# Kernel optimization log

Hardware: AMD Instinct MI355X
Metric: run time of the kernel (lower is better)

The kernel has to match this reference:

```python
import jax, jax.numpy as jnp
import numpy as np

B, H, S, D = 2, 16, 2048, 64
DROPOUT_P = 0.1
INV_SCALE = 8.0  # sqrt(D), original: q.size(3) * k.size(-1)**-0.5


def setup_inputs() -> dict:
    key = jax.random.key(0)
    kq, kk, kv, km = jax.random.split(key, 4)
    query = jax.random.normal(kq, (B, H, S, D), dtype=jnp.float32)
    k_ = jax.random.normal(kk, (B, H, S, D), dtype=jnp.float32)
    value = jax.random.normal(kv, (B, H, S, D), dtype=jnp.float32)
    keep = jax.random.bernoulli(km, 1.0 - DROPOUT_P, (B, H, S, S))
    # torch train-mode dropout: keep-mask scaled by 1/(1-p)
    dropout_mask = keep.astype(jnp.float32) / (1.0 - DROPOUT_P)
    return {"query": query, "key": k_, "value": value, "dropout_mask": dropout_mask}


def reference(query, key, value, dropout_mask):
    # qk = q @ k^T, scaled by 1/sqrt(D)
    scores = jnp.einsum("bhqd,bhkd->bhqk", query, key) / INV_SCALE
    probs = jax.nn.softmax(scores, axis=-1)
    probs = probs * dropout_mask  # deterministic dropout
    out = jnp.einsum("bhqk,bhkd->bhqd", probs, value)
    return out
```

## Files before the change

kernel.cpp:

```cpp
#include <hip/hip_runtime.h>
#include <hip/hip_bf16.h>

typedef __attribute__((ext_vector_type(4))) float f32x4;
typedef __attribute__((ext_vector_type(8))) short s16x8;
typedef __attribute__((ext_vector_type(4))) short s16x4;

constexpr int S    = 2048;
constexpr int D    = 64;
constexpr int BH   = 32;
constexpr int QBLK = 64;
constexpr int KBLK = 32;
constexpr int NSL  = S / KBLK;

__device__ __forceinline__ short f2bf(float f) {
  union { float f; unsigned u; } x;
  x.f = f;
  unsigned r = x.u + 0x7fffu + ((x.u >> 16) & 1u);
  return (short)(r >> 16);
}

typedef const __attribute__((address_space(1))) unsigned int* as1_u32p;
typedef __attribute__((address_space(3))) unsigned int* as3_u32p;

__global__ __launch_bounds__(256) void prepass(const float* __restrict__ K,
                                               const float* __restrict__ V,
                                               short* __restrict__ Kb,
                                               short* __restrict__ Vt) {
  const int bid = blockIdx.x;
  const int tid = threadIdx.x;
  if (bid < BH * 32) {
    const int bh = bid >> 5, sl = bid & 31;
    const float* src = K + ((size_t)bh * S + (size_t)sl * 64) * D;
    short* dst = Kb + ((size_t)bh * S + (size_t)sl * 64) * D;
    #pragma unroll
    for (int c = 0; c < 2; ++c) {
      const int idx = tid * 2 + c;
      const int row = idx >> 3;
      const int ch  = idx & 7;
      const float* s = src + row * D + ch * 8;
      f32x4 a = *(const f32x4*)s, b = *(const f32x4*)(s + 4);
      s16x8 o;
      #pragma unroll
      for (int j = 0; j < 4; ++j) { o[j] = f2bf(a[j]); o[4 + j] = f2bf(b[j]); }
      *(s16x8*)(dst + row * D + ((ch ^ (row & 7)) * 8)) = o;
    }
  } else {
    __shared__ short tile[32][72];
    const int b2 = bid - BH * 32;
    const int bh = b2 >> 6, sl = b2 & 63;
    const float* src = V + ((size_t)bh * S + (size_t)sl * 32) * D;
    {
      const int row = tid >> 3;
      const int c0  = (tid & 7) * 8;
      f32x4 a = *(const f32x4*)(src + row * D + c0);
      f32x4 b = *(const f32x4*)(src + row * D + c0 + 4);
      #pragma unroll
      for (int j = 0; j < 4; ++j) {
        tile[row][c0 + j]     = f2bf(a[j]);
        tile[row][c0 + 4 + j] = f2bf(b[j]);
      }
    }
    __syncthreads();
    short* dst = Vt + ((size_t)bh * 64 + sl) * (D * KBLK);
    const int d = tid >> 2, c = tid & 3;
    const int pos = c ^ ((d >> 1) & 3);
    s16x8 o;
    #pragma unroll
    for (int j = 0; j < 8; ++j) o[j] = tile[c * 8 + j][d];
    *(s16x8*)(dst + d * KBLK + pos * 8) = o;
  }
}

__global__ __launch_bounds__(256, 4)
void attn_fwd3(const float* __restrict__ Qg, const short* __restrict__ Kb,
               const short* __restrict__ Vt, const float* __restrict__ Mg,
               float* __restrict__ Og) {
  __shared__ alignas(16) short K_lds[2][KBLK][64];
  __shared__ alignas(16) short V_lds[2][D][KBLK];
  __shared__ alignas(16) float M_lds[2][QBLK][KBLK];
  __shared__ alignas(16) short P_lds[4][16][KBLK];

  const int tid  = threadIdx.x;
  const int wave = tid >> 6;
  const int lane = tid & 63;
  const int lq   = lane & 15;
  const int g    = lane >> 4;

  const int bh = blockIdx.x & (BH - 1);
  const int qt = blockIdx.x / BH;
  const size_t base = (size_t)bh * S * D;
  const int    qrow = qt * QBLK + wave * 16 + lq;

  s16x8 qf[2];
  {
    const float sc = 1.44269504088896340736f * 0.125f;
    const float* qp = Qg + base + (size_t)qrow * D + g * 8;
    #pragma unroll
    for (int h = 0; h < 2; ++h) {
      f32x4 a = *(const f32x4*)(qp + h * 32);
      f32x4 b = *(const f32x4*)(qp + h * 32 + 4);
      #pragma unroll
      for (int j = 0; j < 4; ++j) {
        qf[h][j]     = f2bf(a[j] * sc);
        qf[h][4 + j] = f2bf(b[j] * sc);
      }
    }
  }

  f32x4 acc[4];
  #pragma unroll
  for (int dt = 0; dt < 4; ++dt) acc[dt] = (f32x4)0.0f;
  float m = -1e30f, lp = 0.0f;

  const char* kbase = (const char*)(Kb + base);
  const char* vbase = (const char*)(Vt + (size_t)bh * 64 * (D * KBLK));
  const char* mblock = (const char*)(Mg + ((size_t)bh * S + (size_t)qt * QBLK) * S);
  char* kl = (char*)&K_lds[0][0][0];
  char* vl = (char*)&V_lds[0][0][0];
  char* ml = (char*)&M_lds[0][0][0];
  char* pl = (char*)&P_lds[wave][lq][0];

  auto stage = [&](int buf, int it) {
    __builtin_amdgcn_global_load_lds((as1_u32p)(kbase + (size_t)it * 4096 + wave * 1024 + lane * 16),
                                     (as3_u32p)(kl + buf * 4096 + wave * 1024 + lane * 16), 16, 0, 0);
    __builtin_amdgcn_global_load_lds((as1_u32p)(vbase + (size_t)it * 4096 + wave * 1024 + lane * 16),
                                     (as3_u32p)(vl + buf * 4096 + wave * 1024 + lane * 16), 16, 0, 0);
    #pragma unroll
    for (int c = 0; c < 2; ++c) {
      const int slot = wave * 2048 + c * 1024 + lane * 16;
      const int q  = slot >> 7;
      const int p  = (slot >> 4) & 7;
      const char* msrc = mblock + (size_t)q * (S * 4) + (size_t)it * (KBLK * 4) + ((p ^ (q & 7)) * 16);
      __builtin_amdgcn_global_load_lds((as1_u32p)msrc, (as3_u32p)(ml + buf * 8192 + slot), 16, 0, 0);
    }
  };

  stage(0, 0);
  __syncthreads();

  int cur = 0;
  for (int it = 0; it < NSL; ++it) {
    if (it + 1 < NSL) stage(cur ^ 1, it + 1);

    f32x4 st[2];
    __builtin_amdgcn_s_setprio(1);
    #pragma unroll
    for (int t = 0; t < 2; ++t) {
      st[t] = (f32x4)0.0f;
      #pragma unroll
      for (int h = 0; h < 2; ++h) {
        const s16x8 kf = *(const s16x8*)(kl + cur * 4096 + (t * 16 + lq) * 128 +
                                         (((h * 4 + g) ^ (lq & 7)) * 16));
        st[t] = __builtin_amdgcn_mfma_f32_16x16x32_bf16(kf, qf[h], st[t], 0, 0, 0);
      }
    }
    __builtin_amdgcn_s_setprio(0);

    const float mx = fmaxf(fmaxf(fmaxf(st[0][0], st[0][1]), fmaxf(st[0][2], st[0][3])),
                           fmaxf(fmaxf(st[1][0], st[1][1]), fmaxf(st[1][2], st[1][3])));
    if (!__all(mx <= m + 8.0f)) {
      float rm = fmaxf(mx, __shfl_xor(mx, 16));
      rm = fmaxf(rm, __shfl_xor(rm, 32));
      const float mn  = fmaxf(m, rm);
      const float fac = __builtin_amdgcn_exp2f(m - mn);
      lp *= fac;
      #pragma unroll
      for (int dt = 0; dt < 4; ++dt)
        #pragma unroll
        for (int r = 0; r < 4; ++r) acc[dt][r] *= fac;
      m = mn;
    }
    float p[8];
    #pragma unroll
    for (int t = 0; t < 2; ++t)
      #pragma unroll
      for (int r = 0; r < 4; ++r) p[t * 4 + r] = __builtin_amdgcn_exp2f(st[t][r] - m);
    lp += ((p[0] + p[1]) + (p[2] + p[3])) + ((p[4] + p[5]) + (p[6] + p[7]));

    #pragma unroll
    for (int t = 0; t < 2; ++t) {
      const f32x4 mk = *(const f32x4*)(ml + cur * 8192 + (wave * 16 + lq) * 128 +
                                       (((t * 4 + g) ^ (lq & 7)) * 16));
      s16x4 pk;
      #pragma unroll
      for (int r = 0; r < 4; ++r) pk[r] = f2bf(p[t * 4 + r] * mk[r]);
      *(s16x4*)(pl + (((2 * t + (g >> 1)) ^ ((lq >> 1) & 3)) * 16) + (g & 1) * 8) = pk;
    }
    asm volatile("" ::: "memory");

    const s16x8 pf = *(const s16x8*)(pl + ((g ^ ((lq >> 1) & 3)) * 16));
    __builtin_amdgcn_s_setprio(1);
    #pragma unroll
    for (int dt = 0; dt < 4; ++dt) {
      const s16x8 vf = *(const s16x8*)(vl + cur * 4096 + (dt * 16 + lq) * 64 +
                                       ((g ^ ((lq >> 1) & 3)) * 16));
      acc[dt] = __builtin_amdgcn_mfma_f32_16x16x32_bf16(vf, pf, acc[dt], 0, 0, 0);
    }
    __builtin_amdgcn_s_setprio(0);

    __syncthreads();
    cur ^= 1;
  }

  float l = lp + __shfl_xor(lp, 16);
  l += __shfl_xor(l, 32);
  const float inv_l = 1.0f / l;
  float* op = Og + base + (size_t)qrow * D;
  #pragma unroll
  for (int dt = 0; dt < 4; ++dt) {
    f32x4 o;
    #pragma unroll
    for (int r = 0; r < 4; ++r) o[r] = acc[dt][r] * inv_l;
    *(f32x4*)(op + dt * 16 + g * 4) = o;
  }
}

__global__ __launch_bounds__(256, 4)
void attn_fwd_fb(const float* __restrict__ Qg, const float* __restrict__ Kg,
                 const float* __restrict__ Vg, const float* __restrict__ Mg,
                 float* __restrict__ Og) {
  __shared__ alignas(16) short Kl[32][72];
  __shared__ alignas(16) short Vl[D][40];
  __shared__ alignas(16) short Pl[4][16][40];
  const int tid = threadIdx.x, wave = tid >> 6, lane = tid & 63;
  const int lq = lane & 15, g = lane >> 4;
  const int bh = blockIdx.x & (BH - 1), qt = blockIdx.x / BH;
  const size_t base = (size_t)bh * S * D;
  const int qrow = qt * QBLK + wave * 16 + lq;
  const float* mrow = Mg + ((size_t)bh * S + qrow) * S;
  s16x8 qf[2];
  {
    const float sc = 1.44269504088896340736f * 0.125f;
    const float* qp = Qg + base + (size_t)qrow * D + g * 8;
    #pragma unroll
    for (int h = 0; h < 2; ++h) {
      f32x4 a = *(const f32x4*)(qp + h * 32);
      f32x4 b = *(const f32x4*)(qp + h * 32 + 4);
      #pragma unroll
      for (int j = 0; j < 4; ++j) { qf[h][j] = f2bf(a[j] * sc); qf[h][4 + j] = f2bf(b[j] * sc); }
    }
  }
  f32x4 acc[4];
  #pragma unroll
  for (int dt = 0; dt < 4; ++dt) acc[dt] = (f32x4)0.0f;
  float m = -1e30f, l = 0.0f;
  for (int kb = 0; kb < S; kb += 32) {
    f32x4 mk[2];
    #pragma unroll
    for (int t = 0; t < 2; ++t) mk[t] = *(const f32x4*)(mrow + kb + t * 16 + g * 4);
    __syncthreads();
    {
      const int row = tid >> 3, d0 = (tid & 7) * 8;
      const float* kp = Kg + base + (size_t)(kb + row) * D + d0;
      f32x4 a = *(const f32x4*)kp, b = *(const f32x4*)(kp + 4);
      s16x8 f;
      #pragma unroll
      for (int j = 0; j < 4; ++j) { f[j] = f2bf(a[j]); f[4 + j] = f2bf(b[j]); }
      *(s16x8*)&Kl[row][d0] = f;
    }
    {
      const int d = tid & 63, kk = (tid >> 6) * 8;
      const float* vp = Vg + base + (size_t)(kb + kk) * D + d;
      s16x8 f;
      #pragma unroll
      for (int j = 0; j < 8; ++j) f[j] = f2bf(vp[(size_t)j * D]);
      *(s16x8*)&Vl[d][kk] = f;
    }
    __syncthreads();
    f32x4 st[2];
    #pragma unroll
    for (int t = 0; t < 2; ++t) {
      st[t] = (f32x4)0.0f;
      #pragma unroll
      for (int h = 0; h < 2; ++h) {
        s16x8 kf = *(const s16x8*)&Kl[t * 16 + lq][h * 32 + g * 8];
        st[t] = __builtin_amdgcn_mfma_f32_16x16x32_bf16(kf, qf[h], st[t], 0, 0, 0);
      }
    }
    float mx = st[0][0];
    #pragma unroll
    for (int t = 0; t < 2; ++t)
      #pragma unroll
      for (int r = 0; r < 4; ++r) mx = fmaxf(mx, st[t][r]);
    mx = fmaxf(mx, __shfl_xor(mx, 16));
    mx = fmaxf(mx, __shfl_xor(mx, 32));
    const float mn = fmaxf(m, mx);
    const float fac = __builtin_amdgcn_exp2f(m - mn);
    float p[8], ps = 0.0f;
    #pragma unroll
    for (int t = 0; t < 2; ++t)
      #pragma unroll
      for (int r = 0; r < 4; ++r) { float e = __builtin_amdgcn_exp2f(st[t][r] - mn); p[t * 4 + r] = e; ps += e; }
    ps += __shfl_xor(ps, 16);
    ps += __shfl_xor(ps, 32);
    l = l * fac + ps; m = mn;
    #pragma unroll
    for (int dt = 0; dt < 4; ++dt)
      #pragma unroll
      for (int r = 0; r < 4; ++r) acc[dt][r] *= fac;
    #pragma unroll
    for (int t = 0; t < 2; ++t) {
      s16x4 pk;
      #pragma unroll
      for (int r = 0; r < 4; ++r) pk[r] = f2bf(p[t * 4 + r] * mk[t][r]);
      *(s16x4*)&Pl[wave][lq][t * 16 + g * 4] = pk;
    }
    asm volatile("" ::: "memory");
    s16x8 pf = *(const s16x8*)&Pl[wave][lq][g * 8];
    #pragma unroll
    for (int dt = 0; dt < 4; ++dt) {
      s16x8 vf = *(const s16x8*)&Vl[dt * 16 + lq][g * 8];
      acc[dt] = __builtin_amdgcn_mfma_f32_16x16x32_bf16(vf, pf, acc[dt], 0, 0, 0);
    }
  }
  const float inv_l = 1.0f / l;
  float* op = Og + base + (size_t)qrow * D;
  #pragma unroll
  for (int dt = 0; dt < 4; ++dt) {
    f32x4 o;
    #pragma unroll
    for (int r = 0; r < 4; ++r) o[r] = acc[dt][r] * inv_l;
    *(f32x4*)(op + dt * 16 + g * 4) = o;
  }
}

extern "C" void kernel_launch(void* const* d_in, const int* in_sizes, int n_in,
                              void* d_out, int out_size, void* d_ws, size_t ws_size,
                              hipStream_t stream) {
  const float* Q = (const float*)d_in[0];
  const float* K = (const float*)d_in[1];
  const float* V = (const float*)d_in[2];
  const float* M = (const float*)d_in[3];
  float* O = (float*)d_out;
  const size_t need = 2ull * BH * S * D * sizeof(short);
  if (ws_size >= need) {
    short* Kb = (short*)d_ws;
    short* Vt = Kb + (size_t)BH * S * D;
    prepass<<<BH * 32 + BH * 64, 256, 0, stream>>>(K, V, Kb, Vt);
    attn_fwd3<<<(S / QBLK) * BH, 256, 0, stream>>>(Q, Kb, Vt, M, O);
  } else {
    attn_fwd_fb<<<(S / QBLK) * BH, 256, 0, stream>>>(Q, K, V, M, O);
  }
}
```

Baseline: 171.1 us.

## Triple-buffer K/V in LDS and load dropout mask directly into registers

The mask is now read straight from global memory into registers one iteration ahead, instead of being staged through LDS. This removes the mask LDS buffers and their LDS traffic. K/V move to a three-deep LDS ring, prefetched two iterations ahead. A manual vmcnt wait plus a bare barrier replaces __syncthreads, and the loop is unrolled by two to ping-pong the mask registers. The manual vmcnt count is fragile, and the global mask loads are only 16B per lane with a row stride, so coalescing may get worse.

```diff
diff --git a/kernel.cpp b/kernel.cpp
--- a/kernel.cpp
+++ b/kernel.cpp
@@ -72,12 +72,11 @@
 }
 
 __global__ __launch_bounds__(256, 4)
-void attn_fwd3(const float* __restrict__ Qg, const short* __restrict__ Kb,
+void attn_fwd4(const float* __restrict__ Qg, const short* __restrict__ Kb,
                const short* __restrict__ Vt, const float* __restrict__ Mg,
                float* __restrict__ Og) {
-  __shared__ alignas(16) short K_lds[2][KBLK][64];
-  __shared__ alignas(16) short V_lds[2][D][KBLK];
-  __shared__ alignas(16) float M_lds[2][QBLK][KBLK];
+  __shared__ alignas(16) short K_lds[3][KBLK][64];
+  __shared__ alignas(16) short V_lds[3][D][KBLK];
   __shared__ alignas(16) short P_lds[4][16][KBLK];
 
   const int tid  = threadIdx.x;
@@ -90,6 +89,7 @@
   const int qt = blockIdx.x / BH;
   const size_t base = (size_t)bh * S * D;
   const int    qrow = qt * QBLK + wave * 16 + lq;
+  const float* mrow = Mg + ((size_t)bh * S + qrow) * S + g * 4;
 
   s16x8 qf[2];
   {
@@ -114,33 +114,28 @@
 
   const char* kbase = (const char*)(Kb + base);
   const char* vbase = (const char*)(Vt + (size_t)bh * 64 * (D * KBLK));
-  const char* mblock = (const char*)(Mg + ((size_t)bh * S + (size_t)qt * QBLK) * S);
   char* kl = (char*)&K_lds[0][0][0];
   char* vl = (char*)&V_lds[0][0][0];
-  char* ml = (char*)&M_lds[0][0][0];
   char* pl = (char*)&P_lds[wave][lq][0];
 
-  auto stage = [&](int buf, int it) {
+  auto stageKV = [&](int buf, int it) {
     __builtin_amdgcn_global_load_lds((as1_u32p)(kbase + (size_t)it * 4096 + wave * 1024 + lane * 16),
                                      (as3_u32p)(kl + buf * 4096 + wave * 1024 + lane * 16), 16, 0, 0);
     __builtin_amdgcn_global_load_lds((as1_u32p)(vbase + (size_t)it * 4096 + wave * 1024 + lane * 16),
                                      (as3_u32p)(vl + buf * 4096 + wave * 1024 + lane * 16), 16, 0, 0);
-    #pragma unroll
-    for (int c = 0; c < 2; ++c) {
-      const int slot = wave * 2048 + c * 1024 + lane * 16;
-      const int q  = slot >> 7;
-      const int p  = (slot >> 4) & 7;
-      const char* msrc = mblock + (size_t)q * (S * 4) + (size_t)it * (KBLK * 4) + ((p ^ (q & 7)) * 16);
-      __builtin_amdgcn_global_load_lds((as1_u32p)msrc, (as3_u32p)(ml + buf * 8192 + slot), 16, 0, 0);
-    }
   };
-
-  stage(0, 0);
-  __syncthreads();
-
-  int cur = 0;
-  for (int it = 0; it < NSL; ++it) {
-    if (it + 1 < NSL) stage(cur ^ 1, it + 1);
+  auto loadM = [&](int it, f32x4* mk) {
+    const float* mp = mrow + it * KBLK;
+    mk[0] = *(const f32x4*)(mp);
+    mk[1] = *(const f32x4*)(mp + 16);
+  };
+
+  auto body = [&](int it, int cur, f32x4* mkU, f32x4* mkN) {
+    {
+      int nb = cur + 2; if (nb >= 3) nb -= 3;
+      if (it + 2 < NSL) stageKV(nb, it + 2);
+      if (it + 1 < NSL) loadM(it + 1, mkN);
+    }
 
     f32x4 st[2];
     __builtin_amdgcn_s_setprio(1);
@@ -179,11 +174,9 @@
 
     #pragma unroll
     for (int t = 0; t < 2; ++t) {
-      const f32x4 mk = *(const f32x4*)(ml + cur * 8192 + (wave * 16 + lq) * 128 +
-                                       (((t * 4 + g) ^ (lq & 7)) * 16));
       s16x4 pk;
       #pragma unroll
-      for (int r = 0; r < 4; ++r) pk[r] = f2bf(p[t * 4 + r] * mk[r]);
+      for (int r = 0; r < 4; ++r) pk[r] = f2bf(p[t * 4 + r] * mkU[t][r]);
       *(s16x4*)(pl + (((2 * t + (g >> 1)) ^ ((lq >> 1) & 3)) * 16) + (g & 1) * 8) = pk;
     }
     asm volatile("" ::: "memory");
@@ -198,8 +191,24 @@
     }
     __builtin_amdgcn_s_setprio(0);
 
-    __syncthreads();
-    cur ^= 1;
+    asm volatile("s_waitcnt vmcnt(4)" ::: "memory");
+    __builtin_amdgcn_s_barrier();
+    __builtin_amdgcn_sched_barrier(0);
+  };
+
+  f32x4 mkA[2], mkB[2];
+  stageKV(0, 0);
+  stageKV(1, 1);
+  loadM(0, mkA);
+  asm volatile("s_waitcnt vmcnt(4)" ::: "memory");
+  __builtin_amdgcn_s_barrier();
+  __builtin_amdgcn_sched_barrier(0);
+
+  int cur = 0;
+  #pragma unroll 1
+  for (int it = 0; it < NSL; it += 2) {
+    body(it,     cur, mkA, mkB); cur = (cur == 2) ? 0 : cur + 1;
+    body(it + 1, cur, mkB, mkA); cur = (cur == 2) ? 0 : cur + 1;
   }
 
   float l = lp + __shfl_xor(lp, 16);
@@ -337,7 +346,7 @@
     short* Kb = (short*)d_ws;
     short* Vt = Kb + (size_t)BH * S * D;
     prepass<<<BH * 32 + BH * 64, 256, 0, stream>>>(K, V, Kb, Vt);
-    attn_fwd3<<<(S / QBLK) * BH, 256, 0, stream>>>(Q, Kb, Vt, M, O);
+    attn_fwd4<<<(S / QBLK) * BH, 256, 0, stream>>>(Q, Kb, Vt, M, O);
   } else {
     attn_fwd_fb<<<(S / QBLK) * BH, 256, 0, stream>>>(Q, K, V, M, O);
   }
```

New measurement: 176.1 us. 2.9% more time.
